# Performance work log

Hardware: AMD Instinct MI355X
Metric: run time of the kernel (lower is better)

The kernel has to match this reference:

```python
import jax, jax.numpy as jnp
import numpy as np

NUM_HEADS = 16

def setup_inputs() -> dict:
    key = jax.random.key(0)
    ks = jax.random.split(key, 7)
    B, N, C, R = 2, 2048, 1024, 64
    s = lambda fan_in: 1.0 / np.sqrt(fan_in)
    return {
        "x": jax.random.normal(ks[0], (B, N, C), dtype=jnp.float32),
        "w_qkv_a": jax.random.uniform(ks[1], (C, R), jnp.float32, -s(C), s(C)),
        "w_qkv_b": jax.random.uniform(ks[2], (R, 3 * C), jnp.float32, -s(R), s(R)),
        "w_proj_a": jax.random.uniform(ks[3], (C, R), jnp.float32, -s(C), s(C)),
        "b_proj_a": jax.random.uniform(ks[4], (R,), jnp.float32, -s(C), s(C)),
        "w_proj_b": jax.random.uniform(ks[5], (R, C), jnp.float32, -s(R), s(R)),
        "b_proj_b": jax.random.uniform(ks[6], (C,), jnp.float32, -s(R), s(R)),
    }

def reference(x, w_qkv_a, w_qkv_b, w_proj_a, b_proj_a, w_proj_b, b_proj_b):
    B, N, C = x.shape
    H = NUM_HEADS
    Dh = C // H
    scale = Dh ** -0.5
    # LoRA QKV: dim -> rank -> 3*dim with exact GELU between (no bias, qkv_bias=False)
    qkv = jax.nn.gelu(x @ w_qkv_a, approximate=False) @ w_qkv_b  # [B,N,3C]
    qkv = qkv.reshape(B, N, 3, H, Dh).transpose(2, 0, 3, 1, 4)  # [3,B,H,N,Dh]
    q, k, v = qkv[0] * scale, qkv[1], qkv[2]
    attn = jax.nn.softmax(jnp.einsum("bhqd,bhkd->bhqk", q, k), axis=-1)
    out = jnp.einsum("bhqk,bhkd->bhqd", attn, v)  # [B,H,N,Dh]
    out = out.transpose(0, 2, 1, 3).reshape(B, N, C)
    # LoRA proj: dim -> rank -> dim with bias (proj_bias=True)
    out = jax.nn.gelu(out @ w_proj_a + b_proj_a, approximate=False) @ w_proj_b + b_proj_b
    return out
```

## Files before the change

kernel.cpp:

```cpp
#include <hip/hip_runtime.h>
#include <cstdint>
#include <cstddef>


typedef short short8 __attribute__((ext_vector_type(8)));
typedef float f32x4 __attribute__((ext_vector_type(4)));

#define MFMA16(a, b, c) __builtin_amdgcn_mfma_f32_16x16x32_bf16((a), (b), (c), 0, 0, 0)

#define QSCALE 0.18033688011112042f

__device__ __forceinline__ float fexp2(float x) { return __builtin_amdgcn_exp2f(x); }

__device__ __forceinline__ uint16_t f2b(float f) {
    return (uint16_t)((__float_as_uint(f) + 0x8000u) >> 16);
}
__device__ __forceinline__ uint32_t pkbf(float a, float b) {
    uint32_t ua = __float_as_uint(a) + 0x8000u;
    uint32_t ub = __float_as_uint(b) + 0x8000u;
    return __builtin_amdgcn_perm(ub, ua, 0x07060302);
}
__device__ __forceinline__ float gelu_exact(float x) {
    return 0.5f * x * (1.0f + erff(x * 0.70710678118654752440f));
}
__device__ __forceinline__ short8 ld8(const uint16_t* p) {
    return *reinterpret_cast<const short8*>(p);
}

__global__ __launch_bounds__(256) void prep(const float* __restrict__ x,
                                            const float* __restrict__ wqa,
                                            const float* __restrict__ wqb,
                                            const float* __restrict__ wpa,
                                            const float* __restrict__ wpb,
                                            uint16_t* __restrict__ xb,
                                            uint16_t* __restrict__ wqaT,
                                            uint16_t* __restrict__ wqbT,
                                            uint16_t* __restrict__ wpaT,
                                            uint16_t* __restrict__ wpbT) {
    const int bid = blockIdx.x;
    if (bid < 2048) {
        size_t i = ((size_t)bid * 256 + threadIdx.x) * 8;
        f32x4 a0 = *reinterpret_cast<const f32x4*>(x + i);
        f32x4 a1 = *reinterpret_cast<const f32x4*>(x + i + 4);
        uint32_t p0 = pkbf(a0[0], a0[1]);
        uint32_t p1 = pkbf(a0[2], a0[3]);
        uint32_t p2 = pkbf(a1[0], a1[1]);
        uint32_t p3 = pkbf(a1[2], a1[3]);
        uint32_t* o = reinterpret_cast<uint32_t*>(xb + i);
        o[0] = p0; o[1] = p1; o[2] = p2; o[3] = p3;
        return;
    }
    int i = (bid - 2048) * 256 + threadIdx.x;
    if (i < 65536) {
        int r = i >> 6, c = i & 63;
        wqaT[(size_t)c * 1024 + r] = f2b(wqa[i]);
    } else if (i < 262144) {
        int j = i - 65536;
        int r = j / 3072, c = j - r * 3072;
        wqbT[(size_t)c * 64 + r] = f2b(wqb[j]);
    } else if (i < 327680) {
        int j = i - 262144;
        int r = j >> 6, c = j & 63;
        wpaT[(size_t)c * 1024 + r] = f2b(wpa[j]);
    } else {
        int j = i - 327680;
        int r = j >> 10, c = j & 1023;
        wpbT[(size_t)c * 64 + r] = f2b(wpb[j]);
    }
}

__global__ __launch_bounds__(256) void rank_gemm(const uint16_t* __restrict__ X,
                                                 const uint16_t* __restrict__ WT,
                                                 const float* __restrict__ bias,
                                                 uint16_t* __restrict__ out) {
    const int wave = threadIdx.x >> 6;
    const int lane = threadIdx.x & 63;
    const int l16 = lane & 15, quad = lane >> 4;
    const int rowg = blockIdx.x;

    const uint16_t* ap = X + (size_t)(rowg * 16 + l16) * 1024 + quad * 8;
    const uint16_t* bp = WT + (size_t)(wave * 16 + l16) * 1024 + quad * 8;

    f32x4 acc = {0.f, 0.f, 0.f, 0.f};
#pragma unroll 8
    for (int k = 0; k < 32; ++k) {
        acc = MFMA16(ld8(ap + k * 32), ld8(bp + k * 32), acc);
    }

    const int col = wave * 16 + l16;
    const float bv = bias ? bias[col] : 0.0f;
#pragma unroll
    for (int r = 0; r < 4; ++r) {
        int row = rowg * 16 + quad * 4 + r;
        out[(size_t)row * 64 + col] = f2b(gelu_exact(acc[r] + bv));
    }
}

__global__ __launch_bounds__(256) void expand_qkv(const uint16_t* __restrict__ H1,
                                                  const uint16_t* __restrict__ WT,
                                                  uint16_t* __restrict__ Qb,
                                                  uint16_t* __restrict__ Kb,
                                                  uint16_t* __restrict__ Vb) {
    const int wave = threadIdx.x >> 6;
    const int lane = threadIdx.x & 63;
    const int l16 = lane & 15, quad = lane >> 4;
    const int wg = blockIdx.x * 4 + wave;
    const int rowg = wg / 48;
    const int colg = wg % 48;

    const uint16_t* ap = H1 + (size_t)(rowg * 16 + l16) * 64 + quad * 8;
    const uint16_t* bp = WT + ((size_t)colg * 64 + l16) * 64 + quad * 8;

    f32x4 acc[4];
#pragma unroll
    for (int c = 0; c < 4; ++c) acc[c] = (f32x4){0.f, 0.f, 0.f, 0.f};

#pragma unroll
    for (int i = 0; i < 2; ++i) {
        short8 a = ld8(ap + i * 32);
#pragma unroll
        for (int c = 0; c < 4; ++c) {
            acc[c] = MFMA16(a, ld8(bp + (size_t)c * 16 * 64 + i * 32), acc[c]);
        }
    }

    const int which = colg >> 4;
    const int h = colg & 15;
#pragma unroll
    for (int c = 0; c < 4; ++c) {
#pragma unroll
        for (int r = 0; r < 4; ++r) {
            int d = c * 16 + l16;
            int row = rowg * 16 + quad * 4 + r;
            int b = row >> 11, n = row & 2047;
            size_t idx = ((size_t)(b * 16 + h) * 2048 + n) * 64 + d;
            float v = acc[c][r];
            if (which == 0) {
                Qb[idx] = f2b(v * QSCALE);
            } else if (which == 1) {
                Kb[idx] = f2b(v);
            } else {
                Vb[idx] = f2b(v);
            }
        }
    }
}

__global__ __launch_bounds__(256) void vtrans(const uint16_t* __restrict__ Vb,
                                              uint16_t* __restrict__ Vtb) {
    __shared__ __align__(16) uint16_t tl[64 * 72];
    const int bh = blockIdx.x >> 5;
    const int nt = blockIdx.x & 31;
    const int r = threadIdx.x >> 2;
    const int c0 = (threadIdx.x & 3) << 4;

    const uint16_t* g = Vb + ((size_t)(bh * 2048 + nt * 64 + r)) * 64 + c0;
    union { short8 v; uint16_t u[8]; } a0, a1;
    a0.v = ld8(g);
    a1.v = ld8(g + 8);
#pragma unroll
    for (int j = 0; j < 8; ++j) {
        tl[(c0 + j) * 72 + r] = a0.u[j];
        tl[(c0 + 8 + j) * 72 + r] = a1.u[j];
    }
    __syncthreads();
    uint16_t* o = Vtb + ((size_t)(bh * 64 + r)) * 2048 + nt * 64 + c0;
    *reinterpret_cast<short8*>(o) = ld8(&tl[r * 72 + c0]);
    *reinterpret_cast<short8*>(o + 8) = ld8(&tl[r * 72 + c0 + 8]);
}

__global__ __launch_bounds__(256, 4) void attn_kernel(const uint16_t* __restrict__ Qb,
                                                      const uint16_t* __restrict__ Kb,
                                                      const uint16_t* __restrict__ Vtb,
                                                      uint16_t* __restrict__ AO) {
    __shared__ __align__(16) uint16_t kt[64 * 72];
    __shared__ __align__(16) uint16_t vt[64 * 72];
    __shared__ __align__(16) uint16_t pl[8 * 16 * 72];

    const int tid = threadIdx.x;
    const int wave = tid >> 6;
    const int lane = tid & 63;
    const int l16 = lane & 15, quad = lane >> 4;
    const int bh = blockIdx.x >> 4;
    const int qg = blockIdx.x & 15;
    const int qbase = qg * 128 + wave * 32;

    short8 qf[2][2];
#pragma unroll
    for (int g = 0; g < 2; ++g) {
        const uint16_t* qp = Qb + ((size_t)(bh * 2048 + qbase + g * 16 + l16)) * 64 + quad * 8;
        qf[g][0] = ld8(qp);
        qf[g][1] = ld8(qp + 32);
    }

    f32x4 o[2][4];
    float l_part[2][4];
#pragma unroll
    for (int g = 0; g < 2; ++g)
#pragma unroll
        for (int c = 0; c < 4; ++c) {
            o[g][c] = (f32x4){0.f, 0.f, 0.f, 0.f};
            l_part[g][c] = 0.f;
        }

    const int sr = tid >> 2;
    const int sc = (tid & 3) << 4;

    for (int t = 0; t < 32; ++t) {
        __syncthreads();
        {
            const uint16_t* kg = Kb + ((size_t)(bh * 2048 + t * 64 + sr)) * 64 + sc;
            *reinterpret_cast<short8*>(&kt[sr * 72 + sc]) = ld8(kg);
            *reinterpret_cast<short8*>(&kt[sr * 72 + sc + 8]) = ld8(kg + 8);
            const uint16_t* vg = Vtb + ((size_t)(bh * 64 + sr)) * 2048 + t * 64 + sc;
            *reinterpret_cast<short8*>(&vt[sr * 72 + sc]) = ld8(vg);
            *reinterpret_cast<short8*>(&vt[sr * 72 + sc + 8]) = ld8(vg + 8);
        }
        __syncthreads();

#pragma unroll
        for (int g = 0; g < 2; ++g) {
            f32x4 s[4];
#pragma unroll
            for (int c = 0; c < 4; ++c) s[c] = (f32x4){0.f, 0.f, 0.f, 0.f};
#pragma unroll
            for (int c = 0; c < 4; ++c) {
                const uint16_t* kp = &kt[(c * 16 + l16) * 72 + quad * 8];
                s[c] = MFMA16(qf[g][0], ld8(kp), s[c]);
                s[c] = MFMA16(qf[g][1], ld8(kp + 32), s[c]);
            }
            uint16_t* pw = &pl[(wave * 2 + g) * 1152];
#pragma unroll
            for (int r = 0; r < 4; ++r) {
                int row = quad * 4 + r;
                float ps = 0.f;
#pragma unroll
                for (int c = 0; c < 4; ++c) {
                    float p = fexp2(s[c][r]);
                    ps += p;
                    pw[row * 72 + c * 16 + l16] = f2b(p);
                }
                l_part[g][r] += ps;
            }
        }
        __builtin_amdgcn_s_waitcnt(0);

#pragma unroll
        for (int g = 0; g < 2; ++g) {
            const uint16_t* pp = &pl[(wave * 2 + g) * 1152 + l16 * 72 + quad * 8];
            const short8 pf0 = ld8(pp);
            const short8 pf1 = ld8(pp + 32);
#pragma unroll
            for (int c = 0; c < 4; ++c) {
                const uint16_t* vp = &vt[(c * 16 + l16) * 72 + quad * 8];
                o[g][c] = MFMA16(pf0, ld8(vp), o[g][c]);
                o[g][c] = MFMA16(pf1, ld8(vp + 32), o[g][c]);
            }
        }
    }

    const int b = bh >> 4, h = bh & 15;
#pragma unroll
    for (int g = 0; g < 2; ++g) {
#pragma unroll
        for (int r = 0; r < 4; ++r) {
            float ls = l_part[g][r];
            ls += __shfl_xor(ls, 1, 64);
            ls += __shfl_xor(ls, 2, 64);
            ls += __shfl_xor(ls, 4, 64);
            ls += __shfl_xor(ls, 8, 64);
            float inv = 1.0f / ls;
            int grow = b * 2048 + qbase + g * 16 + quad * 4 + r;
#pragma unroll
            for (int c = 0; c < 4; ++c) {
                AO[(size_t)grow * 1024 + h * 64 + c * 16 + l16] = f2b(o[g][c][r] * inv);
            }
        }
    }
}

__global__ __launch_bounds__(256) void expand_out(const uint16_t* __restrict__ H2,
                                                  const uint16_t* __restrict__ WT,
                                                  const float* __restrict__ bias,
                                                  float* __restrict__ out) {
    const int wave = threadIdx.x >> 6;
    const int lane = threadIdx.x & 63;
    const int l16 = lane & 15, quad = lane >> 4;
    const int wg = blockIdx.x * 4 + wave;
    const int rowg = wg >> 4;
    const int colg = wg & 15;

    const uint16_t* ap = H2 + (size_t)(rowg * 16 + l16) * 64 + quad * 8;
    const uint16_t* bp = WT + ((size_t)colg * 64 + l16) * 64 + quad * 8;

    f32x4 acc[4];
#pragma unroll
    for (int c = 0; c < 4; ++c) acc[c] = (f32x4){0.f, 0.f, 0.f, 0.f};

#pragma unroll
    for (int i = 0; i < 2; ++i) {
        short8 a = ld8(ap + i * 32);
#pragma unroll
        for (int c = 0; c < 4; ++c) {
            acc[c] = MFMA16(a, ld8(bp + (size_t)c * 16 * 64 + i * 32), acc[c]);
        }
    }

#pragma unroll
    for (int c = 0; c < 4; ++c) {
        int col = colg * 64 + c * 16 + l16;
        float bv = bias[col];
#pragma unroll
        for (int r = 0; r < 4; ++r) {
            int row = rowg * 16 + quad * 4 + r;
            out[(size_t)row * 1024 + col] = acc[c][r] + bv;
        }
    }
}

extern "C" void kernel_launch(void* const* d_in, const int* in_sizes, int n_in,
                              void* d_out, int out_size, void* d_ws, size_t ws_size,
                              hipStream_t stream) {
    const float* x   = (const float*)d_in[0];
    const float* wqa = (const float*)d_in[1];
    const float* wqb = (const float*)d_in[2];
    const float* wpa = (const float*)d_in[3];
    const float* bpa = (const float*)d_in[4];
    const float* wpb = (const float*)d_in[5];
    const float* bpb = (const float*)d_in[6];
    float* out = (float*)d_out;
    uint16_t* ws = (uint16_t*)d_ws;

    uint16_t* wqaT = ws + 0;
    uint16_t* wqbT = ws + 65536;
    uint16_t* wpaT = ws + 262144;
    uint16_t* wpbT = ws + 327680;
    uint16_t* h1   = ws + 393216;
    uint16_t* Qb   = ws + 655360;
    uint16_t* Kb   = ws + 4849664;
    uint16_t* xb   = Kb;
    uint16_t* Vtb  = ws + 9043968;
    uint16_t* AO   = ws + 13238272;
    uint16_t* Vb   = AO;
    uint16_t* h2   = ws + 17432576;
    (void)in_sizes; (void)n_in; (void)out_size; (void)ws_size;

    prep<<<3584, 256, 0, stream>>>(x, wqa, wqb, wpa, wpb, xb, wqaT, wqbT, wpaT, wpbT);
    rank_gemm<<<256, 256, 0, stream>>>(xb, wqaT, nullptr, h1);
    expand_qkv<<<3072, 256, 0, stream>>>(h1, wqbT, Qb, Kb, Vb);
    vtrans<<<1024, 256, 0, stream>>>(Vb, Vtb);
    attn_kernel<<<512, 256, 0, stream>>>(Qb, Kb, Vtb, AO);
    rank_gemm<<<256, 256, 0, stream>>>(AO, wpaT, bpa, h2);
    expand_out<<<1024, 256, 0, stream>>>(h2, wpbT, bpb, out);
}
```

Baseline: 205.1 us.

## Keep softmax probabilities in registers via transposed fp16 PV MFMA and split-K rank GEMM

The attention kernel now computes S transposed (K as the A operand) so each lane's exp'd scores feed the PV MFMA directly as fp16 operands, with V stored as fp16. This removes the per-tile LDS round trip for P and its wait. Each wave now handles 16 query rows and the grid doubles, and output is staged through LDS for vectorized stores. The rank GEMM splits K across two wave groups with an LDS reduction, and the QKV expansion stages its results through LDS so stores are 16-byte vectors. The trade-offs are fp16 precision for P and V, and less Q reuse per K/V tile load.

```diff
diff --git a/kernel.cpp b/kernel.cpp
--- a/kernel.cpp
+++ b/kernel.cpp
@@ -5,8 +5,11 @@
 
 typedef short short8 __attribute__((ext_vector_type(8)));
 typedef float f32x4 __attribute__((ext_vector_type(4)));
+typedef __fp16 half2v __attribute__((ext_vector_type(2)));
+typedef __fp16 half4 __attribute__((ext_vector_type(4)));
 
 #define MFMA16(a, b, c) __builtin_amdgcn_mfma_f32_16x16x32_bf16((a), (b), (c), 0, 0, 0)
+#define MFMA16F(a, b, c) __builtin_amdgcn_mfma_f32_16x16x16f16((a), (b), (c), 0, 0, 0)
 
 #define QSCALE 0.18033688011112042f
 
@@ -19,6 +22,10 @@
     uint32_t ua = __float_as_uint(a) + 0x8000u;
     uint32_t ub = __float_as_uint(b) + 0x8000u;
     return __builtin_amdgcn_perm(ub, ua, 0x07060302);
+}
+__device__ __forceinline__ uint16_t f2h(float f) {
+    half2v t = __builtin_amdgcn_cvt_pkrtz(f, f);
+    return __builtin_bit_cast(uint16_t, t[0]);
 }
 __device__ __forceinline__ float gelu_exact(float x) {
     return 0.5f * x * (1.0f + erff(x * 0.70710678118654752440f));
@@ -42,12 +49,11 @@
         size_t i = ((size_t)bid * 256 + threadIdx.x) * 8;
         f32x4 a0 = *reinterpret_cast<const f32x4*>(x + i);
         f32x4 a1 = *reinterpret_cast<const f32x4*>(x + i + 4);
-        uint32_t p0 = pkbf(a0[0], a0[1]);
-        uint32_t p1 = pkbf(a0[2], a0[3]);
-        uint32_t p2 = pkbf(a1[0], a1[1]);
-        uint32_t p3 = pkbf(a1[2], a1[3]);
         uint32_t* o = reinterpret_cast<uint32_t*>(xb + i);
-        o[0] = p0; o[1] = p1; o[2] = p2; o[3] = p3;
+        o[0] = pkbf(a0[0], a0[1]);
+        o[1] = pkbf(a0[2], a0[3]);
+        o[2] = pkbf(a1[0], a1[1]);
+        o[3] = pkbf(a1[2], a1[3]);
         return;
     }
     int i = (bid - 2048) * 256 + threadIdx.x;
@@ -69,30 +75,40 @@
     }
 }
 
-__global__ __launch_bounds__(256) void rank_gemm(const uint16_t* __restrict__ X,
+__global__ __launch_bounds__(512) void rank_gemm(const uint16_t* __restrict__ X,
                                                  const uint16_t* __restrict__ WT,
                                                  const float* __restrict__ bias,
                                                  uint16_t* __restrict__ out) {
-    const int wave = threadIdx.x >> 6;
-    const int lane = threadIdx.x & 63;
+    __shared__ float ps[4][16][17];
+    const int tid = threadIdx.x;
+    const int wave = tid >> 6, lane = tid & 63;
     const int l16 = lane & 15, quad = lane >> 4;
+    const int cc = wave & 3, kh = wave >> 2;
     const int rowg = blockIdx.x;
 
-    const uint16_t* ap = X + (size_t)(rowg * 16 + l16) * 1024 + quad * 8;
-    const uint16_t* bp = WT + (size_t)(wave * 16 + l16) * 1024 + quad * 8;
+    const uint16_t* ap = X + (size_t)(rowg * 16 + l16) * 1024 + kh * 512 + quad * 8;
+    const uint16_t* bp = WT + (size_t)(cc * 16 + l16) * 1024 + kh * 512 + quad * 8;
 
     f32x4 acc = {0.f, 0.f, 0.f, 0.f};
 #pragma unroll 8
-    for (int k = 0; k < 32; ++k) {
+    for (int k = 0; k < 16; ++k) {
         acc = MFMA16(ld8(ap + k * 32), ld8(bp + k * 32), acc);
     }
 
-    const int col = wave * 16 + l16;
-    const float bv = bias ? bias[col] : 0.0f;
-#pragma unroll
-    for (int r = 0; r < 4; ++r) {
-        int row = rowg * 16 + quad * 4 + r;
-        out[(size_t)row * 64 + col] = f2b(gelu_exact(acc[r] + bv));
+    if (kh == 1) {
+#pragma unroll
+        for (int r = 0; r < 4; ++r) ps[cc][quad * 4 + r][l16] = acc[r];
+    }
+    __syncthreads();
+    if (kh == 0) {
+        const int col = cc * 16 + l16;
+        const float bv = bias ? bias[col] : 0.0f;
+#pragma unroll
+        for (int r = 0; r < 4; ++r) {
+            int row = rowg * 16 + quad * 4 + r;
+            float v = acc[r] + ps[cc][quad * 4 + r][l16] + bv;
+            out[(size_t)row * 64 + col] = f2b(gelu_exact(v));
+        }
     }
 }
 
@@ -101,6 +117,7 @@
                                                   uint16_t* __restrict__ Qb,
                                                   uint16_t* __restrict__ Kb,
                                                   uint16_t* __restrict__ Vb) {
+    __shared__ __align__(16) uint16_t po[4][16 * 72];
     const int wave = threadIdx.x >> 6;
     const int lane = threadIdx.x & 63;
     const int l16 = lane & 15, quad = lane >> 4;
@@ -126,24 +143,25 @@
 
     const int which = colg >> 4;
     const int h = colg & 15;
+    uint16_t* pw = po[wave];
 #pragma unroll
     for (int c = 0; c < 4; ++c) {
 #pragma unroll
         for (int r = 0; r < 4; ++r) {
-            int d = c * 16 + l16;
-            int row = rowg * 16 + quad * 4 + r;
-            int b = row >> 11, n = row & 2047;
-            size_t idx = ((size_t)(b * 16 + h) * 2048 + n) * 64 + d;
             float v = acc[c][r];
-            if (which == 0) {
-                Qb[idx] = f2b(v * QSCALE);
-            } else if (which == 1) {
-                Kb[idx] = f2b(v);
-            } else {
-                Vb[idx] = f2b(v);
-            }
-        }
-    }
+            uint16_t u = (which == 0) ? f2b(v * QSCALE)
+                       : (which == 1) ? f2b(v) : f2h(v);
+            pw[(quad * 4 + r) * 72 + c * 16 + l16] = u;
+        }
+    }
+    __builtin_amdgcn_s_waitcnt(0);
+
+    const int grow = rowg * 16 + l16;
+    const int b = grow >> 11, n = grow & 2047;
+    uint16_t* base = (which == 0) ? Qb : (which == 1) ? Kb : Vb;
+    uint16_t* dst = base + ((size_t)(b * 16 + h) * 2048 + n) * 64 + quad * 16;
+    *reinterpret_cast<short8*>(dst) = ld8(&pw[l16 * 72 + quad * 16]);
+    *reinterpret_cast<short8*>(dst + 8) = ld8(&pw[l16 * 72 + quad * 16 + 8]);
 }
 
 __global__ __launch_bounds__(256) void vtrans(const uint16_t* __restrict__ Vb,
@@ -169,39 +187,29 @@
     *reinterpret_cast<short8*>(o + 8) = ld8(&tl[r * 72 + c0 + 8]);
 }
 
-__global__ __launch_bounds__(256, 4) void attn_kernel(const uint16_t* __restrict__ Qb,
-                                                      const uint16_t* __restrict__ Kb,
-                                                      const uint16_t* __restrict__ Vtb,
-                                                      uint16_t* __restrict__ AO) {
+__global__ __launch_bounds__(256) void attn_kernel(const uint16_t* __restrict__ Qb,
+                                                   const uint16_t* __restrict__ Kb,
+                                                   const uint16_t* __restrict__ Vtb,
+                                                   uint16_t* __restrict__ AO) {
     __shared__ __align__(16) uint16_t kt[64 * 72];
     __shared__ __align__(16) uint16_t vt[64 * 72];
-    __shared__ __align__(16) uint16_t pl[8 * 16 * 72];
 
     const int tid = threadIdx.x;
     const int wave = tid >> 6;
     const int lane = tid & 63;
     const int l16 = lane & 15, quad = lane >> 4;
-    const int bh = blockIdx.x >> 4;
-    const int qg = blockIdx.x & 15;
-    const int qbase = qg * 128 + wave * 32;
-
-    short8 qf[2][2];
-#pragma unroll
-    for (int g = 0; g < 2; ++g) {
-        const uint16_t* qp = Qb + ((size_t)(bh * 2048 + qbase + g * 16 + l16)) * 64 + quad * 8;
-        qf[g][0] = ld8(qp);
-        qf[g][1] = ld8(qp + 32);
-    }
-
-    f32x4 o[2][4];
-    float l_part[2][4];
-#pragma unroll
-    for (int g = 0; g < 2; ++g)
-#pragma unroll
-        for (int c = 0; c < 4; ++c) {
-            o[g][c] = (f32x4){0.f, 0.f, 0.f, 0.f};
-            l_part[g][c] = 0.f;
-        }
+    const int bh = blockIdx.x >> 5;
+    const int qg = blockIdx.x & 31;
+    const int q16 = qg * 64 + wave * 16;
+
+    const uint16_t* qp = Qb + ((size_t)(bh * 2048 + q16 + l16)) * 64 + quad * 8;
+    const short8 qf0 = ld8(qp);
+    const short8 qf1 = ld8(qp + 32);
+
+    f32x4 ot[4];
+#pragma unroll
+    for (int dc = 0; dc < 4; ++dc) ot[dc] = (f32x4){0.f, 0.f, 0.f, 0.f};
+    float lp = 0.f;
 
     const int sr = tid >> 2;
     const int sc = (tid & 3) << 4;
@@ -218,65 +226,51 @@
         }
         __syncthreads();
 
-#pragma unroll
-        for (int g = 0; g < 2; ++g) {
-            f32x4 s[4];
-#pragma unroll
-            for (int c = 0; c < 4; ++c) s[c] = (f32x4){0.f, 0.f, 0.f, 0.f};
-#pragma unroll
-            for (int c = 0; c < 4; ++c) {
-                const uint16_t* kp = &kt[(c * 16 + l16) * 72 + quad * 8];
-                s[c] = MFMA16(qf[g][0], ld8(kp), s[c]);
-                s[c] = MFMA16(qf[g][1], ld8(kp + 32), s[c]);
+        half4 pb[4];
+#pragma unroll
+        for (int kc = 0; kc < 4; ++kc) {
+            const uint16_t* kp = &kt[(kc * 16 + l16) * 72 + quad * 8];
+            f32x4 st = {0.f, 0.f, 0.f, 0.f};
+            st = MFMA16(ld8(kp), qf0, st);
+            st = MFMA16(ld8(kp + 32), qf1, st);
+            float p0 = fexp2(st[0]), p1 = fexp2(st[1]);
+            float p2 = fexp2(st[2]), p3 = fexp2(st[3]);
+            lp += (p0 + p1) + (p2 + p3);
+            half2v lo = __builtin_amdgcn_cvt_pkrtz(p0, p1);
+            half2v hi = __builtin_amdgcn_cvt_pkrtz(p2, p3);
+            pb[kc] = __builtin_shufflevector(lo, hi, 0, 1, 2, 3);
+        }
+
+#pragma unroll
+        for (int dc = 0; dc < 4; ++dc) {
+#pragma unroll
+            for (int kc = 0; kc < 4; ++kc) {
+                const half4 av = *reinterpret_cast<const half4*>(
+                    vt + (dc * 16 + l16) * 72 + kc * 16 + quad * 4);
+                ot[dc] = MFMA16F(av, pb[kc], ot[dc]);
             }
-            uint16_t* pw = &pl[(wave * 2 + g) * 1152];
-#pragma unroll
-            for (int r = 0; r < 4; ++r) {
-                int row = quad * 4 + r;
-                float ps = 0.f;
-#pragma unroll
-                for (int c = 0; c < 4; ++c) {
-                    float p = fexp2(s[c][r]);
-                    ps += p;
-                    pw[row * 72 + c * 16 + l16] = f2b(p);
-                }
-                l_part[g][r] += ps;
-            }
-        }
-        __builtin_amdgcn_s_waitcnt(0);
-
-#pragma unroll
-        for (int g = 0; g < 2; ++g) {
-            const uint16_t* pp = &pl[(wave * 2 + g) * 1152 + l16 * 72 + quad * 8];
-            const short8 pf0 = ld8(pp);
-            const short8 pf1 = ld8(pp + 32);
-#pragma unroll
-            for (int c = 0; c < 4; ++c) {
-                const uint16_t* vp = &vt[(c * 16 + l16) * 72 + quad * 8];
-                o[g][c] = MFMA16(pf0, ld8(vp), o[g][c]);
-                o[g][c] = MFMA16(pf1, ld8(vp + 32), o[g][c]);
-            }
-        }
-    }
+        }
+    }
+
+    lp += __shfl_xor(lp, 16, 64);
+    lp += __shfl_xor(lp, 32, 64);
+    const float inv = 1.0f / lp;
+
+    __syncthreads();
+    uint16_t* pw = &kt[wave * 1152];
+#pragma unroll
+    for (int dc = 0; dc < 4; ++dc) {
+        uint32_t* w = reinterpret_cast<uint32_t*>(&pw[l16 * 72 + dc * 16 + quad * 4]);
+        w[0] = pkbf(ot[dc][0] * inv, ot[dc][1] * inv);
+        w[1] = pkbf(ot[dc][2] * inv, ot[dc][3] * inv);
+    }
+    __builtin_amdgcn_s_waitcnt(0);
 
     const int b = bh >> 4, h = bh & 15;
-#pragma unroll
-    for (int g = 0; g < 2; ++g) {
-#pragma unroll
-        for (int r = 0; r < 4; ++r) {
-            float ls = l_part[g][r];
-            ls += __shfl_xor(ls, 1, 64);
-            ls += __shfl_xor(ls, 2, 64);
-            ls += __shfl_xor(ls, 4, 64);
-            ls += __shfl_xor(ls, 8, 64);
-            float inv = 1.0f / ls;
-            int grow = b * 2048 + qbase + g * 16 + quad * 4 + r;
-#pragma unroll
-            for (int c = 0; c < 4; ++c) {
-                AO[(size_t)grow * 1024 + h * 64 + c * 16 + l16] = f2b(o[g][c][r] * inv);
-            }
-        }
-    }
+    const int grow = b * 2048 + q16 + l16;
+    uint16_t* dst = AO + (size_t)grow * 1024 + h * 64 + quad * 16;
+    *reinterpret_cast<short8*>(dst) = ld8(&pw[l16 * 72 + quad * 16]);
+    *reinterpret_cast<short8*>(dst + 8) = ld8(&pw[l16 * 72 + quad * 16 + 8]);
 }
 
 __global__ __launch_bounds__(256) void expand_out(const uint16_t* __restrict__ H2,
@@ -346,10 +340,10 @@
     (void)in_sizes; (void)n_in; (void)out_size; (void)ws_size;
 
     prep<<<3584, 256, 0, stream>>>(x, wqa, wqb, wpa, wpb, xb, wqaT, wqbT, wpaT, wpbT);
-    rank_gemm<<<256, 256, 0, stream>>>(xb, wqaT, nullptr, h1);
+    rank_gemm<<<256, 512, 0, stream>>>(xb, wqaT, nullptr, h1);
     expand_qkv<<<3072, 256, 0, stream>>>(h1, wqbT, Qb, Kb, Vb);
     vtrans<<<1024, 256, 0, stream>>>(Vb, Vtb);
-    attn_kernel<<<512, 256, 0, stream>>>(Qb, Kb, Vtb, AO);
-    rank_gemm<<<256, 256, 0, stream>>>(AO, wpaT, bpa, h2);
+    attn_kernel<<<1024, 256, 0, stream>>>(Qb, Kb, Vtb, AO);
+    rank_gemm<<<256, 512, 0, stream>>>(AO, wpaT, bpa, h2);
     expand_out<<<1024, 256, 0, stream>>>(h2, wpbT, bpb, out);
 }
```

Measured after the change: 205.2 us. About the same (+0.0%).
